# Kernel optimization log

Hardware: AMD Instinct MI355X
Metric: run time of the kernel (lower is better)

Reference implementation:

```python
import jax, jax.numpy as jnp
import numpy as np

# ---- constants from init_kwargs / module body ----
Z0_MM, DX_MM, DY_MM = 300.0, 1.0, 1.0
IM_SIZE = (-100.0, 100.0, -100.0, 100.0)
KK = 100000
N, M = 512, 512
A, B = 50, 40                      # image grid, hard-coded in forward
BA = A * B
SPEED_OF_LIGHT = 299792458.0
KCONST = 2.0 * np.pi * 77e9 * 2.0 / SPEED_OF_LIGHT   # cst = 1j*KCONST
DI = 0.01


def setup_inputs() -> dict:
    key = jax.random.key(0)
    sar_data = jax.random.normal(key, (N, M), dtype=jnp.float32)
    # sorted subset of kk unique indices out of N*M (matches sorted randperm[:kk])
    rng = np.random.default_rng(0)
    py = np.sort(rng.choice(N * M, size=KK, replace=False)).astype(np.int64)
    return {"sar_data": sar_data, "py": jnp.asarray(py)}


def _build_Hp(py):
    # vectorized replacement of the doubly-nested scalar loop
    iy = (py % N).astype(jnp.float32)          # [NM]
    ix = (py // N).astype(jnp.float32)         # [NM]
    wh1 = jnp.linspace(IM_SIZE[0], IM_SIZE[1], A, dtype=jnp.float32) * 1e-3
    wh2 = jnp.linspace(IM_SIZE[2], IM_SIZE[3], B, dtype=jnp.float32) * 1e-3
    jarr = jnp.arange(BA)
    jy = jarr % B
    jx = jarr // B
    ay = (iy + 0.5 - N / 2) * (DY_MM * 1e-3)   # [NM]
    ax = (ix + 0.5 - M / 2) * (DX_MM * 1e-3)   # [NM]
    z2 = jnp.float32((Z0_MM * 1e-3) ** 2)
    # dist2[i,j] = (ay_i - wh2[jy_j])^2 + (ax_i - wh1[jx_j])^2 + z2
    dist = jnp.sqrt((ay[:, None] - wh2[jy][None, :]) ** 2
                    + (ax[:, None] - wh1[jx][None, :]) ** 2 + z2)  # [NM, BA]
    phase = (KCONST * dist).astype(jnp.float32)
    return jnp.exp(1j * phase).astype(jnp.complex64)   # exp(cst*sqrt(dist2))


def reference(sar_data, py):
    Hp = _build_Hp(py)                                     # [NM, BA] c64
    rd = sar_data.reshape(-1)[py].astype(jnp.complex64)[:, None]  # [NM,1]
    G = DI * (Hp.conj().T @ Hp)                            # [BA, BA]
    xd = DI * (Hp.conj().T @ rd)                           # [BA, 1]

    def step(carry, j):
        G, xd = carry
        col_j = jax.lax.dynamic_index_in_dim(G, j, axis=1, keepdims=False)  # G[:, j]
        temp = col_j / (1.0 + col_j[j])                    # [BA]
        xd = xd - temp[:, None] * xd[j]                    # xd[j] is [1]
        row_j = jax.lax.dynamic_index_in_dim(G, j, axis=0, keepdims=False)  # G[j, :]
        G = G - temp[:, None] * row_j[None, :]
        return (G, xd), None

    (G, xd), _ = jax.lax.scan(step, (G, xd), jnp.arange(BA))
    xd = xd / jnp.diagonal(G)[:, None]
    sar_image = jnp.flip(xd.reshape(B, A), axis=1)
    return sar_image
```

## Files before the change

kernel.cpp:

```cpp
#include <hip/hip_runtime.h>
#include <hip/hip_bf16.h>
#include <stdint.h>

#define KKTOT 100000
#define BAP   2048
#define KPADMAX 100352

typedef _Float16 f16x8 __attribute__((ext_vector_type(8)));
typedef float    f32x4 __attribute__((ext_vector_type(4)));

__device__ __constant__ float KCf  = (float)(4.0 * 3.14159265358979323846 * 77.0e9 / 299792458.0);
__device__ __constant__ float I2PA = (float)(0.15915494309189534940823);
__device__ __constant__ float I2PB = (float)(0.15915494309189534940823 - (double)(float)(0.15915494309189534940823));

__device__ __forceinline__ float phase_frac(float dy, float dxx) {
    float d2 = fmaf(dy, dy, fmaf(dxx, dxx, 0.09f));
    float ph = KCf * sqrtf(d2);
    float h  = ph * I2PA;
    float l  = fmaf(ph, I2PA, -h);
    l = fmaf(ph, I2PB, l);
    return (h - floorf(h)) + l;
}

__device__ __forceinline__ void gload16(const void* g, void* l) {
    __builtin_amdgcn_global_load_lds(
        (__attribute__((address_space(1))) void*)(uintptr_t)g,
        (__attribute__((address_space(3))) void*)(uint32_t)(uintptr_t)l,
        16, 0, 0);
}

__device__ __forceinline__ float2 cmulf(float2 a, float2 b) {
    return make_float2(a.x*b.x - a.y*b.y, a.x*b.y + a.y*b.x);
}

__global__ __launch_bounds__(256) void decode_k(const float* __restrict__ sar, const int* __restrict__ py,
                                                float* __restrict__ ay, float* __restrict__ ax, float* __restrict__ rd) {
    int i = blockIdx.x * 256 + threadIdx.x;
    if (i >= KKTOT) return;
    int p = py[i];
    int iy = p & 511, ix = p >> 9;
    ay[i] = ((float)iy + 0.5f - 256.0f) * 1e-3f;
    ax[i] = ((float)ix + 0.5f - 256.0f) * 1e-3f;
    rd[i] = sar[p];
}

__global__ __launch_bounds__(256) void gen_cs(_Float16* __restrict__ C, _Float16* __restrict__ S,
                                              const float* __restrict__ ay, const float* __restrict__ ax,
                                              int k0, int Kc) {
    int j = blockIdx.y;
    long long kk = ((long long)blockIdx.x * 256 + threadIdx.x) * 8;
    size_t o = (size_t)j * Kc + kk;
    long long kg = (long long)k0 + kk;
    f16x8 cv, sv;
    if (j < 2000 && kg < KKTOT) {
        int jy = j % 40, jx = j / 40;
        float why = ((float)jy * (200.0f/39.0f) - 100.0f) * 1e-3f;
        float whx = ((float)jx * (200.0f/49.0f) - 100.0f) * 1e-3f;
        float4 a0 = *(const float4*)(ay + kg);
        float4 a1 = *(const float4*)(ay + kg + 4);
        float4 b0 = *(const float4*)(ax + kg);
        float4 b1 = *(const float4*)(ax + kg + 4);
        float ayv[8] = {a0.x,a0.y,a0.z,a0.w,a1.x,a1.y,a1.z,a1.w};
        float axv[8] = {b0.x,b0.y,b0.z,b0.w,b1.x,b1.y,b1.z,b1.w};
        #pragma unroll
        for (int e = 0; e < 8; ++e) {
            float fr = phase_frac(ayv[e]-why, axv[e]-whx);
            cv[e] = (_Float16)__builtin_amdgcn_cosf(fr);
            sv[e] = (_Float16)__builtin_amdgcn_sinf(fr);
        }
    } else {
        #pragma unroll
        for (int e = 0; e < 8; ++e) { cv[e] = (_Float16)0.f; sv[e] = (_Float16)0.f; }
    }
    *(f16x8*)(C + o) = cv;
    *(f16x8*)(S + o) = sv;
}

__global__ __launch_bounds__(256) void gemm_ut(const _Float16* __restrict__ C, const _Float16* __restrict__ S,
                                               float* __restrict__ R, float* __restrict__ Pm,
                                               int kiters, int kstride) {
    int rem = blockIdx.x;
    int mi = 0;
    #pragma unroll
    for (int r = 0; r < 16; ++r) {
        int cnt = 16 - r;
        if (rem < cnt) { mi = r; break; }
        rem -= cnt;
    }
    const int ni = mi + rem;
    const int z = blockIdx.y;

    __shared__ _Float16 ldsCa[8192];
    __shared__ _Float16 ldsSa[8192];
    __shared__ _Float16 ldsCb[8192];
    __shared__ _Float16 ldsSb[8192];
    const int t = threadIdx.x;
    const int w = t >> 6;
    const int lane = t & 63;

    f32x4 accR[4][4], accP[4][4];
    #pragma unroll
    for (int a = 0; a < 4; ++a)
        #pragma unroll
        for (int b = 0; b < 4; ++b) { accR[a][b] = (f32x4){0.f,0.f,0.f,0.f}; accP[a][b] = (f32x4){0.f,0.f,0.f,0.f}; }

    size_t aoff[4], boff[4];
    #pragma unroll
    for (int r = 0; r < 4; ++r) {
        int c = r * 256 + t;
        int jl = c >> 3;
        int ks = (c & 7) ^ (jl & 7);
        aoff[r] = (size_t)(mi*128 + jl) * kstride + ks*8;
        boff[r] = (size_t)(ni*128 + jl) * kstride + ks*8;
    }
    const int wm = w & 1, wn = w >> 1;
    const int q = lane >> 4, lm = lane & 15;
    const int ajl = wm*64 + lm;
    const int aoffl = (ajl*8 + (q ^ (ajl & 7))) * 16;
    const int bjl = wn*64 + lm;
    const int boffl = (bjl*8 + (q ^ (bjl & 7))) * 16;

    const int kq = kiters >> 4;
    for (int kt = z*kq; kt < (z+1)*kq; ++kt) {
        __syncthreads();
        const _Float16* gc = C + (size_t)kt * 64;
        const _Float16* gs = S + (size_t)kt * 64;
        #pragma unroll
        for (int r = 0; r < 4; ++r) {
            size_t dst = (size_t)(r*256 + w*64)*16;
            gload16(gc + aoff[r], (char*)ldsCa + dst);
            gload16(gs + aoff[r], (char*)ldsSa + dst);
            gload16(gc + boff[r], (char*)ldsCb + dst);
            gload16(gs + boff[r], (char*)ldsSb + dst);
        }
        __syncthreads();
        #pragma unroll
        for (int ks = 0; ks < 2; ++ks) {
            f16x8 bfC[4], bfS[4];
            #pragma unroll
            for (int nt = 0; nt < 4; ++nt) {
                bfC[nt] = *(const f16x8*)((const char*)ldsCb + ((boffl ^ (ks*64)) + nt*2048));
                bfS[nt] = *(const f16x8*)((const char*)ldsSb + ((boffl ^ (ks*64)) + nt*2048));
            }
            #pragma unroll
            for (int mt = 0; mt < 4; ++mt) {
                f16x8 afC = *(const f16x8*)((const char*)ldsCa + ((aoffl ^ (ks*64)) + mt*2048));
                f16x8 afS = *(const f16x8*)((const char*)ldsSa + ((aoffl ^ (ks*64)) + mt*2048));
                f16x8 nfS;
                #pragma unroll
                for (int e = 0; e < 8; ++e) nfS[e] = -afS[e];
                #pragma unroll
                for (int nt = 0; nt < 4; ++nt) {
                    accR[mt][nt] = __builtin_amdgcn_mfma_f32_16x16x32_f16(afC, bfC[nt], accR[mt][nt], 0, 0, 0);
                    accR[mt][nt] = __builtin_amdgcn_mfma_f32_16x16x32_f16(afS, bfS[nt], accR[mt][nt], 0, 0, 0);
                    accP[mt][nt] = __builtin_amdgcn_mfma_f32_16x16x32_f16(afC, bfS[nt], accP[mt][nt], 0, 0, 0);
                    accP[mt][nt] = __builtin_amdgcn_mfma_f32_16x16x32_f16(nfS, bfC[nt], accP[mt][nt], 0, 0, 0);
                }
            }
        }
    }
    #pragma unroll
    for (int mt = 0; mt < 4; ++mt) {
        #pragma unroll
        for (int nt = 0; nt < 4; ++nt) {
            int row0 = mi*128 + wm*64 + mt*16 + q*4;
            int col  = ni*128 + wn*64 + nt*16 + lm;
            float* rp = R  + (size_t)row0 * BAP + col;
            float* pp = Pm + (size_t)row0 * BAP + col;
            #pragma unroll
            for (int rr = 0; rr < 4; ++rr) {
                atomicAdd(rp + (size_t)rr * BAP, accR[mt][nt][rr]);
                atomicAdd(pp + (size_t)rr * BAP, accP[mt][nt][rr]);
            }
        }
    }
}

__global__ __launch_bounds__(256) void xd_init(const float* __restrict__ ay, const float* __restrict__ ax,
                                               const float* __restrict__ rd, float2* __restrict__ xd) {
    int j = blockIdx.x;
    int t = threadIdx.x;
    __shared__ float redr[256], redi[256];
    if (j >= 2000) { if (t == 0) xd[j] = make_float2(0.f, 0.f); return; }
    int jy = j % 40, jx = j / 40;
    float why = ((float)jy * (200.0f/39.0f) - 100.0f) * 1e-3f;
    float whx = ((float)jx * (200.0f/49.0f) - 100.0f) * 1e-3f;
    float sr = 0.f, si = 0.f;
    for (int i = t; i < KKTOT; i += 256) {
        float fr = phase_frac(ay[i]-why, ax[i]-whx);
        float r = rd[i];
        sr = fmaf(r, __builtin_amdgcn_cosf(fr), sr);
        si = fmaf(r, __builtin_amdgcn_sinf(fr), si);
    }
    redr[t] = sr; redi[t] = si;
    __syncthreads();
    for (int s2 = 128; s2 > 0; s2 >>= 1) {
        if (t < s2) { redr[t] += redr[t+s2]; redi[t] += redi[t+s2]; }
        __syncthreads();
    }
    if (t == 0) xd[j] = make_float2(0.01f * redr[0], -0.01f * redi[0]);
}

__global__ __launch_bounds__(256) void build_G_tile(const float* __restrict__ R, const float* __restrict__ Pm,
                                                    float2* __restrict__ G) {
    int ti = blockIdx.y, tj = blockIdx.x;
    if (tj < ti) return;
    __shared__ float2 tile[64][65];
    int t = threadIdx.x;
    #pragma unroll
    for (int r = 0; r < 16; ++r) {
        int e = t + 256*r;
        int lr = e >> 6, lc = e & 63;
        size_t mn = (size_t)(ti*64 + lr) * BAP + tj*64 + lc;
        float re = 0.01f * R[mn];
        float im = 0.01f * Pm[mn];
        G[mn] = make_float2(re, im);
        tile[lc][lr] = make_float2(re, -im);
    }
    if (tj == ti) return;
    __syncthreads();
    #pragma unroll
    for (int r = 0; r < 16; ++r) {
        int e = t + 256*r;
        int lr = e >> 6, lc = e & 63;
        G[(size_t)(tj*64 + lr) * BAP + ti*64 + lc] = tile[lr][lc];
    }
}

__global__ __launch_bounds__(256) void panel_factor(const float2* __restrict__ G, const float2* __restrict__ xd,
                                                    float2* __restrict__ Vout, float2* __restrict__ vv,
                                                    float* __restrict__ sarr, int p0) {
    __shared__ float2 Rcm[64*65];
    __shared__ float2 Vcm[64*65];
    __shared__ float2 xdp[64];
    __shared__ float2 dinvv[64];
    int t = threadIdx.x;
    int i = t & 63, cg = t >> 6;
    #pragma unroll
    for (int r = 0; r < 16; ++r) {
        int e = t + 256*r;
        int ci = e & 63, ri = e >> 6;
        Rcm[ci*65 + ri] = G[(size_t)(p0+ri)*BAP + p0 + ci];
    }
    #pragma unroll
    for (int r = 0; r < 17; ++r) {
        int e = t + 256*r;
        if (e < 64*65) Vcm[e] = make_float2(0.f, 0.f);
    }
    if (cg == 0) xdp[i] = xd[p0 + i];
    __syncthreads();

    for (int sub = 0; sub < 4; ++sub) {
        int cS = sub*16 + cg*4;
        float2 raccR[4], raccV[4];
        #pragma unroll
        for (int u = 0; u < 4; ++u) {
            raccR[u] = Rcm[(cS+u)*65 + i];
            raccV[u] = Vcm[(cS+u)*65 + i];
        }
        for (int j = 0; j < sub*16; ++j) {
            float2 dv = dinvv[j];
            float2 colji = Rcm[j*65 + i];
            float2 tj = cmulf(colji, dv);
            float2 vji = Vcm[j*65 + i];
            #pragma unroll
            for (int u = 0; u < 4; ++u) {
                float2 x = Rcm[j*65 + cS + u];
                float2 rv = make_float2(x.x, -x.y);
                raccR[u].x -= tj.x*rv.x - tj.y*rv.y;
                raccR[u].y -= tj.x*rv.y + tj.y*rv.x;
                raccV[u].x += vji.x*rv.x - vji.y*rv.y;
                raccV[u].y += vji.x*rv.y + vji.y*rv.x;
            }
        }
        #pragma unroll
        for (int u = 0; u < 4; ++u) {
            Rcm[(cS+u)*65 + i] = raccR[u];
            Vcm[(cS+u)*65 + i] = raccV[u];
        }
        __syncthreads();
        for (int jj = 0; jj < 16; ++jj) {
            int j = sub*16 + jj;
            float2 pr = Rcm[j*65 + j];
            float dr = 1.0f + pr.x, dii = pr.y;
            float idn = 1.0f / (dr*dr + dii*dii);
            float2 dv = make_float2(dr*idn, -dii*idn);
            float2 colv = Rcm[j*65 + i];
            float2 tp = cmulf(colv, dv);
            float2 mv = Vcm[j*65 + i];
            float2 Vij = cmulf(make_float2((i==j ? 1.0f : 0.0f) - mv.x, -mv.y), dv);
            float2 vj = xdp[j];
            float2 rowv[4];
            #pragma unroll
            for (int u = 0; u < 4; ++u) {
                float2 x = Rcm[j*65 + cS + u];
                rowv[u] = make_float2(x.x, -x.y);
            }
            __syncthreads();
            if (cg == 0) {
                Vcm[j*65 + i] = Vij;
                float2 xi = xdp[i];
                xi.x -= tp.x*vj.x - tp.y*vj.y;
                xi.y -= tp.x*vj.y + tp.y*vj.x;
                xdp[i] = xi;
            }
            if (t == j) { dinvv[j] = dv; vv[j] = vj; sarr[j] = dr; }
            #pragma unroll
            for (int u = 0; u < 4; ++u) {
                int c = cS + u;
                if (c > j) {
                    float2 rv = rowv[u];
                    float2 cur = Rcm[c*65 + i];
                    cur.x -= tp.x*rv.x - tp.y*rv.y;
                    cur.y -= tp.x*rv.y + tp.y*rv.x;
                    Rcm[c*65 + i] = cur;
                    float2 m = Vcm[c*65 + i];
                    m.x += Vij.x*rv.x - Vij.y*rv.y;
                    m.y += Vij.x*rv.y + Vij.y*rv.x;
                    Vcm[c*65 + i] = m;
                }
            }
            __syncthreads();
        }
    }
    #pragma unroll
    for (int r = 0; r < 16; ++r) {
        int e = t + 256*r;
        int ri = e >> 6, ci = e & 63;
        Vout[e] = Vcm[ci*65 + ri];
    }
}

__global__ __launch_bounds__(256) void panel_T(const float2* __restrict__ G, float2* __restrict__ xd,
                                               float2* __restrict__ T,
                                               const float2* __restrict__ V, const float2* __restrict__ vv, int p0) {
    __shared__ float srcRe[64][64];
    __shared__ float srcIm[64][64];
    __shared__ float2 Vb[64*64];
    __shared__ float2 vb[64];
    __shared__ float2 xred[4][64];
    int t = threadIdx.x;
    int ri = t & 63, cg = t >> 6;
    int r = blockIdx.x * 64 + ri;
    {
        const float2* gp = G + (size_t)r * BAP + p0 + cg*16;
        #pragma unroll
        for (int k = 0; k < 16; ++k) {
            float2 g = gp[k];
            srcRe[cg*16 + k][ri] = g.x;
            srcIm[cg*16 + k][ri] = g.y;
        }
    }
    #pragma unroll
    for (int q = 0; q < 16; ++q) {
        int e = t + 256*q;
        Vb[e] = V[e];
    }
    if (cg == 0) vb[ri] = vv[ri];
    __syncthreads();
    int jb = cg * 16;
    float2 acc[16];
    #pragma unroll
    for (int jj = 0; jj < 16; ++jj) acc[jj] = make_float2(0.f, 0.f);
    for (int k = 0; k < 64; ++k) {
        float sx = srcRe[k][ri];
        float sy = srcIm[k][ri];
        #pragma unroll
        for (int jj = 0; jj < 16; ++jj) {
            float2 vk = Vb[k*64 + jb + jj];
            acc[jj].x = fmaf(sx, vk.x, fmaf(-sy, vk.y, acc[jj].x));
            acc[jj].y = fmaf(sx, vk.y, fmaf( sy, vk.x, acc[jj].y));
        }
    }
    float2 xp = make_float2(0.f, 0.f);
    #pragma unroll
    for (int jj = 0; jj < 16; ++jj) {
        T[(size_t)(jb + jj) * BAP + r] = acc[jj];
        float2 vj = vb[jb + jj];
        xp.x += acc[jj].x*vj.x - acc[jj].y*vj.y;
        xp.y += acc[jj].x*vj.y + acc[jj].y*vj.x;
    }
    xred[cg][ri] = xp;
    __syncthreads();
    if (cg == 0) {
        float2 x = xd[r];
        #pragma unroll
        for (int g = 0; g < 4; ++g) { x.x -= xred[g][ri].x; x.y -= xred[g][ri].y; }
        xd[r] = x;
    }
}

__global__ __launch_bounds__(256) void trailing_update(float2* __restrict__ G,
                                                       const float2* __restrict__ T, const float* __restrict__ s,
                                                       int coff, int jmax) {
    if (blockIdx.x == gridDim.x - 1) {
        int j = blockIdx.y * 128 + (threadIdx.x & 127);
        if (threadIdx.x < 128 && j < jmax) {
            float acc = 0.f;
            for (int k = 0; k < 64; ++k) {
                float2 tv = T[(size_t)k * BAP + j];
                acc = fmaf(s[k], fmaf(tv.x, tv.x, tv.y*tv.y), acc);
            }
            size_t jj2 = (size_t)j * BAP + j;
            float2 g = G[jj2];
            g.x -= acc;
            G[jj2] = g;
        }
        return;
    }
    __shared__ float2 Tb[16][128];
    __shared__ float2 Wb[16][64];
    int t = threadIdx.x;
    int cx = (blockIdx.x + coff) * 64, ry = blockIdx.y * 128;
    int rq = t >> 4, cq = t & 15;
    float2 acc[8][4];
    #pragma unroll
    for (int si = 0; si < 8; ++si)
        #pragma unroll
        for (int u = 0; u < 4; ++u) acc[si][u] = make_float2(0.f, 0.f);

    for (int k0 = 0; k0 < 64; k0 += 16) {
        __syncthreads();
        #pragma unroll
        for (int r = 0; r < 4; ++r) {
            int e = t + 256*r;
            int k = e >> 6, x4 = e & 63;
            *(float4*)&Tb[k][x4*2] = *(const float4*)(T + (size_t)(k0+k) * BAP + ry + x4*2);
        }
        #pragma unroll
        for (int r = 0; r < 2; ++r) {
            int e = t + 256*r;
            int k = e >> 5, x4 = e & 31;
            float sk = s[k0+k];
            float4 tv = *(const float4*)(T + (size_t)(k0+k) * BAP + cx + x4*2);
            Wb[k][x4*2]   = make_float2(tv.x*sk, -tv.y*sk);
            Wb[k][x4*2+1] = make_float2(tv.z*sk, -tv.w*sk);
        }
        __syncthreads();
        #pragma unroll
        for (int k = 0; k < 16; ++k) {
            float2 av[8], bv[4];
            #pragma unroll
            for (int si = 0; si < 8; ++si) av[si] = Tb[k][rq + 16*si];
            #pragma unroll
            for (int u = 0; u < 4; ++u) bv[u] = Wb[k][cq + 16*u];
            #pragma unroll
            for (int si = 0; si < 8; ++si)
                #pragma unroll
                for (int u = 0; u < 4; ++u) {
                    acc[si][u].x = fmaf(av[si].x, bv[u].x, fmaf(-av[si].y, bv[u].y, acc[si][u].x));
                    acc[si][u].y = fmaf(av[si].x, bv[u].y, fmaf( av[si].y, bv[u].x, acc[si][u].y));
                }
        }
    }
    #pragma unroll
    for (int si = 0; si < 8; ++si) {
        float2* gp = G + (size_t)(ry + rq + 16*si) * BAP + cx + cq;
        #pragma unroll
        for (int u = 0; u < 4; ++u) {
            float2 gg = gp[16*u];
            gg.x -= acc[si][u].x;
            gg.y -= acc[si][u].y;
            gp[16*u] = gg;
        }
    }
}

__global__ __launch_bounds__(256) void finalize_k(const float2* __restrict__ G, const float2* __restrict__ xd,
                                                  float* __restrict__ out, int out_size) {
    int o = blockIdx.x * 256 + threadIdx.x;
    if (o >= 2000) return;
    int b = o / 50, a = o % 50;
    int j = b * 50 + (49 - a);
    float2 x = xd[j];
    float2 g = G[(size_t)j * BAP + j];
    float den = 1.0f / (g.x*g.x + g.y*g.y);
    float re = (x.x*g.x + x.y*g.y) * den;
    float im = (x.y*g.x - x.x*g.y) * den;
    out[o] = re;
    if (out_size >= 4000) out[2000 + o] = im;
}

extern "C" void kernel_launch(void* const* d_in, const int* in_sizes, int n_in,
                              void* d_out, int out_size, void* d_ws, size_t ws_size,
                              hipStream_t stream) {
    const float* sar = (const float*)d_in[0];
    const int*   py  = (const int*)d_in[1];
    float* out = (float*)d_out;
    char* w = (char*)d_ws;
    size_t off = 0;
    auto take = [&](size_t sz) -> char* { char* p = w + off; off += (sz + 255) & ~(size_t)255; return p; };

    float*  R   = (float*)take((size_t)BAP*BAP*4);
    float*  Pm  = (float*)take((size_t)BAP*BAP*4);
    float2* G  = (float2*)take((size_t)BAP*BAP*8);
    float2* T  = (float2*)take((size_t)64*BAP*8);
    float2* xd = (float2*)take((size_t)BAP*8);
    float*  ay = (float*)take((size_t)KPADMAX*4);
    float*  ax = (float*)take((size_t)KPADMAX*4);
    float*  rd = (float*)take((size_t)KPADMAX*4);
    float2* Vp = (float2*)take(64*64*8);
    float2* vv   = (float2*)take(64*8);
    float*  sarr = (float*)take(64*4);

    size_t avail = (ws_size > off + 4096) ? (ws_size - off - 4096) : 0;
    long long Kc = (long long)(avail / 8192) & ~2047LL;
    if (Kc > KPADMAX) Kc = KPADMAX;
    if (Kc < 2048) Kc = 2048;
    int nch = (int)((KKTOT + Kc - 1) / Kc);
    long long Kc2 = 2048LL * ((KKTOT + (long long)nch*2048 - 1) / ((long long)nch*2048));
    if (Kc2 >= 2048 && Kc2 <= Kc) Kc = Kc2;
    _Float16* C = (_Float16*)take((size_t)BAP * Kc * 2);
    _Float16* S = (_Float16*)take((size_t)BAP * Kc * 2);
    int kiters = (int)(Kc / 64);

    hipMemsetAsync(R, 0, (size_t)BAP*BAP*4*2, stream);

    decode_k<<<dim3(391), dim3(256), 0, stream>>>(sar, py, ay, ax, rd);
    xd_init<<<dim3(BAP), dim3(256), 0, stream>>>(ay, ax, rd, xd);

    for (int c0 = 0; c0 < nch; ++c0) {
        gen_cs<<<dim3((unsigned)(Kc/2048), BAP), dim3(256), 0, stream>>>(C, S, ay, ax, (int)(c0*Kc), (int)Kc);
        gemm_ut<<<dim3(136, 16), dim3(256), 0, stream>>>(C, S, R, Pm, kiters, (int)Kc);
    }
    build_G_tile<<<dim3(32, 32), dim3(256), 0, stream>>>(R, Pm, G);

    for (int p = 0; p < 32; ++p) {
        int p0 = p * 64;
        panel_factor<<<dim3(1), dim3(256), 0, stream>>>(G, xd, Vp, vv, sarr, p0);
        panel_T<<<dim3(32), dim3(256), 0, stream>>>(G, xd, T, Vp, vv, p0);
        trailing_update<<<dim3(32 - p, 16), dim3(256), 0, stream>>>(G, T, sarr, p + 1, p0 + 64);
    }
    finalize_k<<<dim3(8), dim3(256), 0, stream>>>(G, xd, out, out_size);
}
```

Before: 5.982 ms.

## Fuse panel factor, T and trailing update into one persistent kernel with grid barriers

Replaces the 96 per-panel kernel launches with a single persistent kernel of 256 blocks that loops over all 32 panels. Stages are separated by a software grid barrier built on atomics, and work is distributed across blocks with strided loops. This removes launch overhead and inter-kernel gaps. In exchange it relies on all 256 blocks being co-resident, uses 68 KB of shared memory per block, and adds barrier spin cost.

```diff
diff --git a/kernel.cpp b/kernel.cpp
--- a/kernel.cpp
+++ b/kernel.cpp
@@ -5,6 +5,7 @@
 #define KKTOT 100000
 #define BAP   2048
 #define KPADMAX 100352
+#define NBLK  256
 
 typedef _Float16 f16x8 __attribute__((ext_vector_type(8)));
 typedef float    f32x4 __attribute__((ext_vector_type(4)));
@@ -31,6 +32,23 @@
 
 __device__ __forceinline__ float2 cmulf(float2 a, float2 b) {
     return make_float2(a.x*b.x - a.y*b.y, a.x*b.y + a.y*b.x);
+}
+
+__device__ __forceinline__ void grid_barrier(int* __restrict__ bar) {
+    __syncthreads();
+    __threadfence();
+    if (threadIdx.x == 0) {
+        int gen = atomicAdd(&bar[1], 0);
+        int t = atomicAdd(&bar[0], 1);
+        if (t == NBLK - 1) {
+            atomicExch(&bar[0], 0);
+            atomicAdd(&bar[1], 1);
+        } else {
+            while (atomicAdd(&bar[1], 0) == gen) __builtin_amdgcn_s_sleep(2);
+        }
+    }
+    __syncthreads();
+    __threadfence();
 }
 
 __global__ __launch_bounds__(256) void decode_k(const float* __restrict__ sar, const int* __restrict__ py,
@@ -227,242 +245,250 @@
     }
 }
 
-__global__ __launch_bounds__(256) void panel_factor(const float2* __restrict__ G, const float2* __restrict__ xd,
-                                                    float2* __restrict__ Vout, float2* __restrict__ vv,
-                                                    float* __restrict__ sarr, int p0) {
-    __shared__ float2 Rcm[64*65];
-    __shared__ float2 Vcm[64*65];
-    __shared__ float2 xdp[64];
-    __shared__ float2 dinvv[64];
-    int t = threadIdx.x;
-    int i = t & 63, cg = t >> 6;
-    #pragma unroll
-    for (int r = 0; r < 16; ++r) {
-        int e = t + 256*r;
-        int ci = e & 63, ri = e >> 6;
-        Rcm[ci*65 + ri] = G[(size_t)(p0+ri)*BAP + p0 + ci];
-    }
-    #pragma unroll
-    for (int r = 0; r < 17; ++r) {
-        int e = t + 256*r;
-        if (e < 64*65) Vcm[e] = make_float2(0.f, 0.f);
-    }
-    if (cg == 0) xdp[i] = xd[p0 + i];
-    __syncthreads();
-
-    for (int sub = 0; sub < 4; ++sub) {
-        int cS = sub*16 + cg*4;
-        float2 raccR[4], raccV[4];
-        #pragma unroll
-        for (int u = 0; u < 4; ++u) {
-            raccR[u] = Rcm[(cS+u)*65 + i];
-            raccV[u] = Vcm[(cS+u)*65 + i];
-        }
-        for (int j = 0; j < sub*16; ++j) {
-            float2 dv = dinvv[j];
-            float2 colji = Rcm[j*65 + i];
-            float2 tj = cmulf(colji, dv);
-            float2 vji = Vcm[j*65 + i];
-            #pragma unroll
-            for (int u = 0; u < 4; ++u) {
-                float2 x = Rcm[j*65 + cS + u];
-                float2 rv = make_float2(x.x, -x.y);
-                raccR[u].x -= tj.x*rv.x - tj.y*rv.y;
-                raccR[u].y -= tj.x*rv.y + tj.y*rv.x;
-                raccV[u].x += vji.x*rv.x - vji.y*rv.y;
-                raccV[u].y += vji.x*rv.y + vji.y*rv.x;
-            }
-        }
-        #pragma unroll
-        for (int u = 0; u < 4; ++u) {
-            Rcm[(cS+u)*65 + i] = raccR[u];
-            Vcm[(cS+u)*65 + i] = raccV[u];
-        }
-        __syncthreads();
-        for (int jj = 0; jj < 16; ++jj) {
-            int j = sub*16 + jj;
-            float2 pr = Rcm[j*65 + j];
-            float dr = 1.0f + pr.x, dii = pr.y;
-            float idn = 1.0f / (dr*dr + dii*dii);
-            float2 dv = make_float2(dr*idn, -dii*idn);
-            float2 colv = Rcm[j*65 + i];
-            float2 tp = cmulf(colv, dv);
-            float2 mv = Vcm[j*65 + i];
-            float2 Vij = cmulf(make_float2((i==j ? 1.0f : 0.0f) - mv.x, -mv.y), dv);
-            float2 vj = xdp[j];
-            float2 rowv[4];
-            #pragma unroll
-            for (int u = 0; u < 4; ++u) {
-                float2 x = Rcm[j*65 + cS + u];
-                rowv[u] = make_float2(x.x, -x.y);
-            }
+__global__ __launch_bounds__(256) void chain_k(float2* __restrict__ G, float2* __restrict__ xd,
+                                               float2* __restrict__ T, float2* __restrict__ Vp,
+                                               float2* __restrict__ vvv, float* __restrict__ sarr,
+                                               int* __restrict__ bar) {
+    __shared__ __align__(16) char smem[69632];
+    const int bid = blockIdx.x;
+    const int t = threadIdx.x;
+    const int i = t & 63, wg = t >> 6;
+
+    for (int p = 0; p < 32; ++p) {
+        const int p0 = p * 64;
+        if (bid == 0) {
+            float2* Rcm   = (float2*)smem;
+            float2* Vcm   = Rcm + 64*65;
+            float2* xdp   = Vcm + 64*65;
+            float2* dinvv = xdp + 64;
+            #pragma unroll
+            for (int r = 0; r < 16; ++r) {
+                int e = t + 256*r;
+                int ci = e & 63, ri = e >> 6;
+                Rcm[ci*65 + ri] = G[(size_t)(p0+ri)*BAP + p0 + ci];
+            }
+            #pragma unroll
+            for (int r = 0; r < 17; ++r) {
+                int e = t + 256*r;
+                if (e < 64*65) Vcm[e] = make_float2(0.f, 0.f);
+            }
+            if (wg == 0) xdp[i] = xd[p0 + i];
             __syncthreads();
-            if (cg == 0) {
-                Vcm[j*65 + i] = Vij;
-                float2 xi = xdp[i];
-                xi.x -= tp.x*vj.x - tp.y*vj.y;
-                xi.y -= tp.x*vj.y + tp.y*vj.x;
-                xdp[i] = xi;
-            }
-            if (t == j) { dinvv[j] = dv; vv[j] = vj; sarr[j] = dr; }
-            #pragma unroll
-            for (int u = 0; u < 4; ++u) {
-                int c = cS + u;
-                if (c > j) {
-                    float2 rv = rowv[u];
-                    float2 cur = Rcm[c*65 + i];
-                    cur.x -= tp.x*rv.x - tp.y*rv.y;
-                    cur.y -= tp.x*rv.y + tp.y*rv.x;
-                    Rcm[c*65 + i] = cur;
-                    float2 m = Vcm[c*65 + i];
-                    m.x += Vij.x*rv.x - Vij.y*rv.y;
-                    m.y += Vij.x*rv.y + Vij.y*rv.x;
-                    Vcm[c*65 + i] = m;
-                }
-            }
+            for (int sub = 0; sub < 4; ++sub) {
+                int cS = sub*16 + wg*4;
+                float2 raccR[4], raccV[4];
+                #pragma unroll
+                for (int u = 0; u < 4; ++u) {
+                    raccR[u] = Rcm[(cS+u)*65 + i];
+                    raccV[u] = Vcm[(cS+u)*65 + i];
+                }
+                for (int j = 0; j < sub*16; ++j) {
+                    float2 dv = dinvv[j];
+                    float2 colji = Rcm[j*65 + i];
+                    float2 tj = cmulf(colji, dv);
+                    float2 vji = Vcm[j*65 + i];
+                    #pragma unroll
+                    for (int u = 0; u < 4; ++u) {
+                        float2 x = Rcm[j*65 + cS + u];
+                        float2 rv = make_float2(x.x, -x.y);
+                        raccR[u].x -= tj.x*rv.x - tj.y*rv.y;
+                        raccR[u].y -= tj.x*rv.y + tj.y*rv.x;
+                        raccV[u].x += vji.x*rv.x - vji.y*rv.y;
+                        raccV[u].y += vji.x*rv.y + vji.y*rv.x;
+                    }
+                }
+                #pragma unroll
+                for (int u = 0; u < 4; ++u) {
+                    Rcm[(cS+u)*65 + i] = raccR[u];
+                    Vcm[(cS+u)*65 + i] = raccV[u];
+                }
+                __syncthreads();
+                for (int jj = 0; jj < 16; ++jj) {
+                    int j = sub*16 + jj;
+                    float2 pr = Rcm[j*65 + j];
+                    float dr = 1.0f + pr.x, dii = pr.y;
+                    float idn = 1.0f / (dr*dr + dii*dii);
+                    float2 dv = make_float2(dr*idn, -dii*idn);
+                    float2 colv = Rcm[j*65 + i];
+                    float2 tp = cmulf(colv, dv);
+                    float2 mv = Vcm[j*65 + i];
+                    float2 Vij = cmulf(make_float2((i==j ? 1.0f : 0.0f) - mv.x, -mv.y), dv);
+                    float2 vj = xdp[j];
+                    float2 rowv[4];
+                    #pragma unroll
+                    for (int u = 0; u < 4; ++u) {
+                        float2 x = Rcm[j*65 + cS + u];
+                        rowv[u] = make_float2(x.x, -x.y);
+                    }
+                    __syncthreads();
+                    if (wg == 0) {
+                        Vcm[j*65 + i] = Vij;
+                        float2 xi = xdp[i];
+                        xi.x -= tp.x*vj.x - tp.y*vj.y;
+                        xi.y -= tp.x*vj.y + tp.y*vj.x;
+                        xdp[i] = xi;
+                    }
+                    if (t == j) { dinvv[j] = dv; vvv[j] = vj; sarr[j] = dr; }
+                    #pragma unroll
+                    for (int u = 0; u < 4; ++u) {
+                        int c = cS + u;
+                        if (c > j) {
+                            float2 rv = rowv[u];
+                            float2 cur = Rcm[c*65 + i];
+                            cur.x -= tp.x*rv.x - tp.y*rv.y;
+                            cur.y -= tp.x*rv.y + tp.y*rv.x;
+                            Rcm[c*65 + i] = cur;
+                            float2 m = Vcm[c*65 + i];
+                            m.x += Vij.x*rv.x - Vij.y*rv.y;
+                            m.y += Vij.x*rv.y + Vij.y*rv.x;
+                            Vcm[c*65 + i] = m;
+                        }
+                    }
+                    __syncthreads();
+                }
+            }
+            #pragma unroll
+            for (int r = 0; r < 16; ++r) {
+                int e = t + 256*r;
+                int ri = e >> 6, ci = e & 63;
+                Vp[e] = Vcm[ci*65 + ri];
+            }
+        }
+        grid_barrier(bar);
+        for (int rt = bid; rt < 32; rt += NBLK) {
+            float*  srcRe = (float*)smem;
+            float*  srcIm = srcRe + 4096;
+            float2* Vb    = (float2*)(srcIm + 4096);
+            float2* vb    = Vb + 4096;
+            float2* xred  = vb + 64;
+            int r = rt * 64 + i;
+            {
+                const float2* gp = G + (size_t)r * BAP + p0 + wg*16;
+                #pragma unroll
+                for (int k = 0; k < 16; ++k) {
+                    float2 g = gp[k];
+                    srcRe[(wg*16 + k)*64 + i] = g.x;
+                    srcIm[(wg*16 + k)*64 + i] = g.y;
+                }
+            }
+            #pragma unroll
+            for (int q = 0; q < 16; ++q) {
+                int e = t + 256*q;
+                Vb[e] = Vp[e];
+            }
+            if (wg == 0) vb[i] = vvv[i];
             __syncthreads();
-        }
-    }
-    #pragma unroll
-    for (int r = 0; r < 16; ++r) {
-        int e = t + 256*r;
-        int ri = e >> 6, ci = e & 63;
-        Vout[e] = Vcm[ci*65 + ri];
-    }
-}
-
-__global__ __launch_bounds__(256) void panel_T(const float2* __restrict__ G, float2* __restrict__ xd,
-                                               float2* __restrict__ T,
-                                               const float2* __restrict__ V, const float2* __restrict__ vv, int p0) {
-    __shared__ float srcRe[64][64];
-    __shared__ float srcIm[64][64];
-    __shared__ float2 Vb[64*64];
-    __shared__ float2 vb[64];
-    __shared__ float2 xred[4][64];
-    int t = threadIdx.x;
-    int ri = t & 63, cg = t >> 6;
-    int r = blockIdx.x * 64 + ri;
-    {
-        const float2* gp = G + (size_t)r * BAP + p0 + cg*16;
-        #pragma unroll
-        for (int k = 0; k < 16; ++k) {
-            float2 g = gp[k];
-            srcRe[cg*16 + k][ri] = g.x;
-            srcIm[cg*16 + k][ri] = g.y;
-        }
-    }
-    #pragma unroll
-    for (int q = 0; q < 16; ++q) {
-        int e = t + 256*q;
-        Vb[e] = V[e];
-    }
-    if (cg == 0) vb[ri] = vv[ri];
-    __syncthreads();
-    int jb = cg * 16;
-    float2 acc[16];
-    #pragma unroll
-    for (int jj = 0; jj < 16; ++jj) acc[jj] = make_float2(0.f, 0.f);
-    for (int k = 0; k < 64; ++k) {
-        float sx = srcRe[k][ri];
-        float sy = srcIm[k][ri];
-        #pragma unroll
-        for (int jj = 0; jj < 16; ++jj) {
-            float2 vk = Vb[k*64 + jb + jj];
-            acc[jj].x = fmaf(sx, vk.x, fmaf(-sy, vk.y, acc[jj].x));
-            acc[jj].y = fmaf(sx, vk.y, fmaf( sy, vk.x, acc[jj].y));
-        }
-    }
-    float2 xp = make_float2(0.f, 0.f);
-    #pragma unroll
-    for (int jj = 0; jj < 16; ++jj) {
-        T[(size_t)(jb + jj) * BAP + r] = acc[jj];
-        float2 vj = vb[jb + jj];
-        xp.x += acc[jj].x*vj.x - acc[jj].y*vj.y;
-        xp.y += acc[jj].x*vj.y + acc[jj].y*vj.x;
-    }
-    xred[cg][ri] = xp;
-    __syncthreads();
-    if (cg == 0) {
-        float2 x = xd[r];
-        #pragma unroll
-        for (int g = 0; g < 4; ++g) { x.x -= xred[g][ri].x; x.y -= xred[g][ri].y; }
-        xd[r] = x;
-    }
-}
-
-__global__ __launch_bounds__(256) void trailing_update(float2* __restrict__ G,
-                                                       const float2* __restrict__ T, const float* __restrict__ s,
-                                                       int coff, int jmax) {
-    if (blockIdx.x == gridDim.x - 1) {
-        int j = blockIdx.y * 128 + (threadIdx.x & 127);
-        if (threadIdx.x < 128 && j < jmax) {
-            float acc = 0.f;
+            int jb = wg * 16;
+            float2 acc[16];
+            #pragma unroll
+            for (int jj = 0; jj < 16; ++jj) acc[jj] = make_float2(0.f, 0.f);
             for (int k = 0; k < 64; ++k) {
-                float2 tv = T[(size_t)k * BAP + j];
-                acc = fmaf(s[k], fmaf(tv.x, tv.x, tv.y*tv.y), acc);
-            }
-            size_t jj2 = (size_t)j * BAP + j;
-            float2 g = G[jj2];
-            g.x -= acc;
-            G[jj2] = g;
-        }
-        return;
-    }
-    __shared__ float2 Tb[16][128];
-    __shared__ float2 Wb[16][64];
-    int t = threadIdx.x;
-    int cx = (blockIdx.x + coff) * 64, ry = blockIdx.y * 128;
-    int rq = t >> 4, cq = t & 15;
-    float2 acc[8][4];
-    #pragma unroll
-    for (int si = 0; si < 8; ++si)
-        #pragma unroll
-        for (int u = 0; u < 4; ++u) acc[si][u] = make_float2(0.f, 0.f);
-
-    for (int k0 = 0; k0 < 64; k0 += 16) {
-        __syncthreads();
-        #pragma unroll
-        for (int r = 0; r < 4; ++r) {
-            int e = t + 256*r;
-            int k = e >> 6, x4 = e & 63;
-            *(float4*)&Tb[k][x4*2] = *(const float4*)(T + (size_t)(k0+k) * BAP + ry + x4*2);
-        }
-        #pragma unroll
-        for (int r = 0; r < 2; ++r) {
-            int e = t + 256*r;
-            int k = e >> 5, x4 = e & 31;
-            float sk = s[k0+k];
-            float4 tv = *(const float4*)(T + (size_t)(k0+k) * BAP + cx + x4*2);
-            Wb[k][x4*2]   = make_float2(tv.x*sk, -tv.y*sk);
-            Wb[k][x4*2+1] = make_float2(tv.z*sk, -tv.w*sk);
-        }
-        __syncthreads();
-        #pragma unroll
-        for (int k = 0; k < 16; ++k) {
-            float2 av[8], bv[4];
-            #pragma unroll
-            for (int si = 0; si < 8; ++si) av[si] = Tb[k][rq + 16*si];
-            #pragma unroll
-            for (int u = 0; u < 4; ++u) bv[u] = Wb[k][cq + 16*u];
-            #pragma unroll
-            for (int si = 0; si < 8; ++si)
-                #pragma unroll
-                for (int u = 0; u < 4; ++u) {
-                    acc[si][u].x = fmaf(av[si].x, bv[u].x, fmaf(-av[si].y, bv[u].y, acc[si][u].x));
-                    acc[si][u].y = fmaf(av[si].x, bv[u].y, fmaf( av[si].y, bv[u].x, acc[si][u].y));
-                }
-        }
-    }
-    #pragma unroll
-    for (int si = 0; si < 8; ++si) {
-        float2* gp = G + (size_t)(ry + rq + 16*si) * BAP + cx + cq;
-        #pragma unroll
-        for (int u = 0; u < 4; ++u) {
-            float2 gg = gp[16*u];
-            gg.x -= acc[si][u].x;
-            gg.y -= acc[si][u].y;
-            gp[16*u] = gg;
-        }
+                float sx = srcRe[k*64 + i];
+                float sy = srcIm[k*64 + i];
+                #pragma unroll
+                for (int jj = 0; jj < 16; ++jj) {
+                    float2 vk = Vb[k*64 + jb + jj];
+                    acc[jj].x = fmaf(sx, vk.x, fmaf(-sy, vk.y, acc[jj].x));
+                    acc[jj].y = fmaf(sx, vk.y, fmaf( sy, vk.x, acc[jj].y));
+                }
+            }
+            float2 xp = make_float2(0.f, 0.f);
+            #pragma unroll
+            for (int jj = 0; jj < 16; ++jj) {
+                T[(size_t)(jb + jj) * BAP + r] = acc[jj];
+                float2 vj = vb[jb + jj];
+                xp.x += acc[jj].x*vj.x - acc[jj].y*vj.y;
+                xp.y += acc[jj].x*vj.y + acc[jj].y*vj.x;
+            }
+            xred[wg*64 + i] = xp;
+            __syncthreads();
+            if (wg == 0) {
+                float2 x = xd[r];
+                #pragma unroll
+                for (int g2 = 0; g2 < 4; ++g2) { x.x -= xred[g2*64 + i].x; x.y -= xred[g2*64 + i].y; }
+                xd[r] = x;
+            }
+            __syncthreads();
+        }
+        grid_barrier(bar);
+        {
+            int nct = (31 - p) * 16;
+            for (int wk = bid; wk < nct + 16; wk += NBLK) {
+                if (wk < nct) {
+                    float2* Tb = (float2*)smem;
+                    float2* Wb = Tb + 16*128;
+                    int cidx = wk >> 4, ridx = wk & 15;
+                    int cx = (p + 1 + cidx) * 64, ry = ridx * 128;
+                    int rq = t >> 4, cq = t & 15;
+                    float2 acc[8][4];
+                    #pragma unroll
+                    for (int si = 0; si < 8; ++si)
+                        #pragma unroll
+                        for (int u = 0; u < 4; ++u) acc[si][u] = make_float2(0.f, 0.f);
+                    for (int k0 = 0; k0 < 64; k0 += 16) {
+                        __syncthreads();
+                        #pragma unroll
+                        for (int r = 0; r < 4; ++r) {
+                            int e = t + 256*r;
+                            int k = e >> 6, x4 = e & 63;
+                            *(float4*)&Tb[k*128 + x4*2] = *(const float4*)(T + (size_t)(k0+k) * BAP + ry + x4*2);
+                        }
+                        #pragma unroll
+                        for (int r = 0; r < 2; ++r) {
+                            int e = t + 256*r;
+                            int k = e >> 5, x4 = e & 31;
+                            float sk = sarr[k0+k];
+                            float4 tv = *(const float4*)(T + (size_t)(k0+k) * BAP + cx + x4*2);
+                            Wb[k*64 + x4*2]   = make_float2(tv.x*sk, -tv.y*sk);
+                            Wb[k*64 + x4*2+1] = make_float2(tv.z*sk, -tv.w*sk);
+                        }
+                        __syncthreads();
+                        #pragma unroll
+                        for (int k = 0; k < 16; ++k) {
+                            float2 av[8], bv[4];
+                            #pragma unroll
+                            for (int si = 0; si < 8; ++si) av[si] = Tb[k*128 + rq + 16*si];
+                            #pragma unroll
+                            for (int u = 0; u < 4; ++u) bv[u] = Wb[k*64 + cq + 16*u];
+                            #pragma unroll
+                            for (int si = 0; si < 8; ++si)
+                                #pragma unroll
+                                for (int u = 0; u < 4; ++u) {
+                                    acc[si][u].x = fmaf(av[si].x, bv[u].x, fmaf(-av[si].y, bv[u].y, acc[si][u].x));
+                                    acc[si][u].y = fmaf(av[si].x, bv[u].y, fmaf( av[si].y, bv[u].x, acc[si][u].y));
+                                }
+                        }
+                    }
+                    #pragma unroll
+                    for (int si = 0; si < 8; ++si) {
+                        float2* gp = G + (size_t)(ry + rq + 16*si) * BAP + cx + cq;
+                        #pragma unroll
+                        for (int u = 0; u < 4; ++u) {
+                            float2 gg = gp[16*u];
+                            gg.x -= acc[si][u].x;
+                            gg.y -= acc[si][u].y;
+                            gp[16*u] = gg;
+                        }
+                    }
+                    __syncthreads();
+                } else {
+                    int d = wk - nct;
+                    int j = d * 128 + (t & 127);
+                    if (t < 128 && j < p0 + 64) {
+                        float acc2 = 0.f;
+                        for (int k = 0; k < 64; ++k) {
+                            float2 tv = T[(size_t)k * BAP + j];
+                            acc2 = fmaf(sarr[k], fmaf(tv.x, tv.x, tv.y*tv.y), acc2);
+                        }
+                        size_t jj2 = (size_t)j * BAP + j;
+                        float2 g = G[jj2];
+                        g.x -= acc2;
+                        G[jj2] = g;
+                    }
+                }
+            }
+        }
+        grid_barrier(bar);
     }
 }
 
@@ -502,6 +528,7 @@
     float2* Vp = (float2*)take(64*64*8);
     float2* vv   = (float2*)take(64*8);
     float*  sarr = (float*)take(64*4);
+    int*    bar  = (int*)take(256);
 
     size_t avail = (ws_size > off + 4096) ? (ws_size - off - 4096) : 0;
     long long Kc = (long long)(avail / 8192) & ~2047LL;
@@ -515,6 +542,7 @@
     int kiters = (int)(Kc / 64);
 
     hipMemsetAsync(R, 0, (size_t)BAP*BAP*4*2, stream);
+    hipMemsetAsync(bar, 0, 256, stream);
 
     decode_k<<<dim3(391), dim3(256), 0, stream>>>(sar, py, ay, ax, rd);
     xd_init<<<dim3(BAP), dim3(256), 0, stream>>>(ay, ax, rd, xd);
@@ -525,11 +553,7 @@
     }
     build_G_tile<<<dim3(32, 32), dim3(256), 0, stream>>>(R, Pm, G);
 
-    for (int p = 0; p < 32; ++p) {
-        int p0 = p * 64;
-        panel_factor<<<dim3(1), dim3(256), 0, stream>>>(G, xd, Vp, vv, sarr, p0);
-        panel_T<<<dim3(32), dim3(256), 0, stream>>>(G, xd, T, Vp, vv, p0);
-        trailing_update<<<dim3(32 - p, 16), dim3(256), 0, stream>>>(G, T, sarr, p + 1, p0 + 64);
-    }
+    chain_k<<<dim3(NBLK), dim3(256), 0, stream>>>(G, xd, T, Vp, vv, sarr, bar);
+
     finalize_k<<<dim3(8), dim3(256), 0, stream>>>(G, xd, out, out_size);
 }
```

New measurement: 9.550 ms. +59.6%, slower.
